# Kernel optimization log

Measured on AMD Instinct MI355X. Metric: run time of the kernel, lower is better.

Reference implementation:

```python
import jax, jax.numpy as jnp
import numpy as np


def setup_inputs() -> dict:
    key = jax.random.key(0)
    ks = jax.random.split(key, 8)
    B, dz, K, N, dx, T = 64, 16, 16, 1024, 128, 500
    # initial latent state [n_trials, dz, k_particles]
    z0 = jax.random.normal(ks[0], (B, dz, K), jnp.float32)
    # per-latent leak/time-constant A = (1 - dt/tau), kept in (0.8, 0.99) for stability
    A = jax.random.uniform(ks[1], (dz,), jnp.float32, minval=0.8, maxval=0.99)
    # low-rank recurrent factors: n [dz, N] (right), m [N, dz] (left)
    n = jax.random.normal(ks[2], (dz, N), jnp.float32) * (1.0 / N)
    m = jax.random.normal(ks[3], (N, dz), jnp.float32) * (1.0 / np.sqrt(dz))
    # neuron bias h [N], latent bias hz [dz]
    h = jax.random.normal(ks[4], (N,), jnp.float32) * 0.1
    hz = jax.random.normal(ks[5], (dz,), jnp.float32) * 0.01
    # readout B [dz, dx] ~ sqrt(2/dy) randn, bias initialised to zero (as in Observation)
    Bobs = jax.random.normal(ks[6], (dz, dx), jnp.float32) * np.sqrt(2.0 / dz)
    Bias = jnp.zeros((dx,), jnp.float32)
    return {"z0": z0, "A": A, "n": n, "m": m, "h": h, "hz": hz,
            "Bobs": Bobs, "Bias": Bias, "T": T}


def reference(z0, A, n, m, h, hz, Bobs, Bias, T):
    """Low-rank RNN rolled out for T steps + linear (identity-nonlin) readout.

    Per step (Transition.forward with relu nonlinearity, weight_scaler=1, du=0):
        R   = relu(m @ z - h)                       # rates, [B, N, K]
        z'  = A * z + n @ R + hz                    # [B, dz, K]
    Readout (Observation.forward, identity nonlinearity):
        X = einsum('zx,bzTK->bxTK', Bobs, zs) + Bias
    """
    Ab = A[None, :, None]      # [1, dz, 1]
    hb = h[None, :, None]      # [1, N, 1]
    hzb = hz[None, :, None]    # [1, dz, 1]

    def step(z, _):
        X = jnp.einsum('Nz,bzk->bNk', m, z)           # project to neurons
        R = jax.nn.relu(X - hb)                       # rates
        z_new = Ab * z + jnp.einsum('zN,bNk->bzk', n, R) + hzb
        return z_new, z_new

    _, zs = jax.lax.scan(step, z0, None, length=T)    # [T, B, dz, K]
    zs = jnp.transpose(zs, (1, 2, 0, 3))              # [B, dz, T, K]
    # Observation readout
    X = jnp.einsum('zx,bzTK->bxTK', Bobs, zs) + Bias[None, :, None, None]
    return X
```

## Files before the change

kernel.cpp:

```cpp
#include <hip/hip_runtime.h>
#include <hip/hip_bf16.h>


typedef __attribute__((ext_vector_type(4))) short short4v;
typedef __attribute__((ext_vector_type(8))) short short8v;
typedef __attribute__((ext_vector_type(4))) float float4v;

#define BB 64
#define DZ 16
#define KC 16
#define NN 1024
#define DX 128
#define NW 8
#define ITER (NN / (16 * NW))
#define NH (ITER / 2)
#define CH 8

union FragAB {
  short4v s;
  __hip_bfloat162 h2[2];
};
union Frag8 {
  short8v s8;
  short4v s4[2];
};

__device__ inline short4v pack_bf16x4(float a, float b, float c, float d) {
  FragAB u;
  u.h2[0] = __float22bfloat162_rn(make_float2(a, b));
  u.h2[1] = __float22bfloat162_rn(make_float2(c, d));
  return u.s;
}

__device__ inline float4v mfma_bf16(short4v a, short4v b, float4v c) {
#if __has_builtin(__builtin_amdgcn_mfma_f32_16x16x16bf16_1k)
  return __builtin_amdgcn_mfma_f32_16x16x16bf16_1k(a, b, c, 0, 0, 0);
#elif __has_builtin(__builtin_amdgcn_mfma_f32_16x16x16_bf16)
  return __builtin_amdgcn_mfma_f32_16x16x16_bf16(a, b, c, 0, 0, 0);
#else
  float4v d;
  asm("v_mfma_f32_16x16x16_bf16 %0, %1, %2, %3"
      : "=v"(d) : "v"(a), "v"(b), "v"(c));
  return d;
#endif
}

__device__ inline float4v mfma_bf16_x32(short8v a, short8v b, float4v c) {
#if __has_builtin(__builtin_amdgcn_mfma_f32_16x16x32_bf16)
  return __builtin_amdgcn_mfma_f32_16x16x32_bf16(a, b, c, 0, 0, 0);
#else
  float4v d;
  asm("v_mfma_f32_16x16x32_bf16 %0, %1, %2, %3"
      : "=v"(d) : "v"(a), "v"(b), "v"(c));
  return d;
#endif
}

__global__ __launch_bounds__(64 * NW, 2)
void lrrnn_fused(const float* __restrict__ z0, const float* __restrict__ Adec,
                 const float* __restrict__ nmat, const float* __restrict__ mmat,
                 const float* __restrict__ hvec, const float* __restrict__ hzvec,
                 const float* __restrict__ Bobs, const float* __restrict__ Bias,
                 const int* __restrict__ Tptr, float* __restrict__ out)
{
  const int T    = Tptr[0];
  const int b    = blockIdx.x;
  const int tid  = threadIdx.x;
  const int wave = tid >> 6;
  const int lane = tid & 63;
  const int g    = lane >> 4;
  const int c    = lane & 15;

  __shared__ float4v part[NW][64];
  __shared__ short4v zbuf[64];

  FragAB mf[ITER];
  Frag8  nf8[NH];
  float4v negH[ITER];
#pragma unroll
  for (int i = 0; i < ITER; ++i) {
    const int rowbase = wave * (16 * ITER) + i * 16;
    float4v mv = *(const float4v*)(mmat + (rowbase + c) * DZ + g * 4);
    mf[i].s = pack_bf16x4(mv[0], mv[1], mv[2], mv[3]);
    float4v hv = *(const float4v*)(hvec + rowbase + g * 4);
    negH[i][0] = -hv[0]; negH[i][1] = -hv[1];
    negH[i][2] = -hv[2]; negH[i][3] = -hv[3];
  }
#pragma unroll
  for (int i = 0; i < NH; ++i) {
    const int rb0 = wave * (16 * ITER) + (2 * i) * 16;
    float4v nv0 = *(const float4v*)(nmat + c * NN + rb0 + g * 4);
    float4v nv1 = *(const float4v*)(nmat + c * NN + rb0 + 16 + g * 4);
    nf8[i].s4[0] = pack_bf16x4(nv0[0], nv0[1], nv0[2], nv0[3]);
    nf8[i].s4[1] = pack_bf16x4(nv1[0], nv1[1], nv1[2], nv1[3]);
  }

  const float4v Af  = *(const float4v*)(Adec + g * 4);
  const float4v hzf = *(const float4v*)(hzvec + g * 4);
  const float4v zerov = {0.f, 0.f, 0.f, 0.f};

  FragAB bobsF;
  float4v biasF;
  unsigned oof[4];
  {
    const int xb = wave * 16;
    bobsF.s = pack_bf16x4(Bobs[(4 * g + 0) * DX + xb + c],
                          Bobs[(4 * g + 1) * DX + xb + c],
                          Bobs[(4 * g + 2) * DX + xb + c],
                          Bobs[(4 * g + 3) * DX + xb + c]);
    biasF = *(const float4v*)(Bias + xb + g * 4);
#pragma unroll
    for (int rr = 0; rr < 4; ++rr) {
      const int x = xb + g * 4 + rr;
      oof[rr] = (unsigned)(b * DX + x) * (unsigned)T * KC + c;
    }
  }

  float4v zf;
#pragma unroll
  for (int j = 0; j < 4; ++j)
    zf[j] = z0[b * DZ * KC + (g * 4 + j) * KC + c];
  FragAB zb;
  zb.s = pack_bf16x4(zf[0], zf[1], zf[2], zf[3]);

  auto do_step = [&]() {
    float4v xv[ITER];
#pragma unroll
    for (int i = 0; i < ITER; ++i)
      xv[i] = mfma_bf16(mf[i].s, zb.s, negH[i]);

    Frag8 R8[NH];
#pragma unroll
    for (int i = 0; i < NH; ++i) {
      const float4v x0 = xv[2 * i], x1 = xv[2 * i + 1];
      R8[i].s4[0] = pack_bf16x4(fmaxf(x0[0], 0.f), fmaxf(x0[1], 0.f),
                                fmaxf(x0[2], 0.f), fmaxf(x0[3], 0.f));
      R8[i].s4[1] = pack_bf16x4(fmaxf(x1[0], 0.f), fmaxf(x1[1], 0.f),
                                fmaxf(x1[2], 0.f), fmaxf(x1[3], 0.f));
    }

    float4v a0 = mfma_bf16_x32(nf8[0].s8, R8[0].s8, (wave == 0) ? hzf : zerov);
    float4v a1 = mfma_bf16_x32(nf8[1].s8, R8[1].s8, zerov);
    a0 = mfma_bf16_x32(nf8[2].s8, R8[2].s8, a0);
    a1 = mfma_bf16_x32(nf8[3].s8, R8[3].s8, a1);
    const float4v zp = a0 + a1;

    part[wave][lane] = zp;
    __syncthreads();

    if (wave == 0) {
      const float4v p1 = part[1][lane];
      const float4v p2 = part[2][lane];
      const float4v p3 = part[3][lane];
      const float4v p4 = part[4][lane];
      const float4v p5 = part[5][lane];
      const float4v p6 = part[6][lane];
      const float4v p7 = part[7][lane];
      const float4v tot = ((zp + p1) + (p2 + p3)) + ((p4 + p5) + (p6 + p7));
#pragma unroll
      for (int j = 0; j < 4; ++j)
        zf[j] = fmaf(Af[j], zf[j], tot[j]);
      zb.s = pack_bf16x4(zf[0], zf[1], zf[2], zf[3]);
      zbuf[lane] = zb.s;
    }
    __syncthreads();

    if (wave != 0) zb.s = zbuf[lane];
  };

  int t = 0;
  while (t + CH <= T) {
    short4v hist[CH];
#pragma unroll
    for (int s = 0; s < CH; ++s) {
      do_step();
      hist[s] = zb.s;
    }
#pragma unroll
    for (int s = 0; s < CH; ++s) {
      float4v o = mfma_bf16(bobsF.s, hist[s], biasF);
      const unsigned tk = (unsigned)(t + s) * KC;
#pragma unroll
      for (int rr = 0; rr < 4; ++rr)
        out[oof[rr] + tk] = o[rr];
    }
    t += CH;
  }
  for (; t < T; ++t) {
    do_step();
    float4v o = mfma_bf16(bobsF.s, zb.s, biasF);
    const unsigned tk = (unsigned)t * KC;
#pragma unroll
    for (int rr = 0; rr < 4; ++rr)
      out[oof[rr] + tk] = o[rr];
  }
}

extern "C" void kernel_launch(void* const* d_in, const int* in_sizes, int n_in,
                              void* d_out, int out_size, void* d_ws, size_t ws_size,
                              hipStream_t stream) {
  const float* z0   = (const float*)d_in[0];
  const float* A    = (const float*)d_in[1];
  const float* nmat = (const float*)d_in[2];
  const float* mmat = (const float*)d_in[3];
  const float* h    = (const float*)d_in[4];
  const float* hz   = (const float*)d_in[5];
  const float* Bobs = (const float*)d_in[6];
  const float* Bias = (const float*)d_in[7];
  const int*   T    = (const int*)d_in[8];
  (void)in_sizes; (void)n_in; (void)out_size; (void)d_ws; (void)ws_size;
  lrrnn_fused<<<dim3(BB), dim3(64 * NW), 0, stream>>>(
      z0, A, nmat, mmat, h, hz, Bobs, Bias, T, (float*)d_out);
}
```

Before: 343.9 us.

## Replace two-barrier reduction with redundant all-wave reduction and double-buffered partials

Every wave now reads all eight partial sums from shared memory and computes the updated latent state itself, instead of wave 0 reducing and broadcasting through a second shared buffer. Double-buffering the partial array lets each step use a single barrier rather than two. The decay and bias term is computed before the MFMA chain so it stays off the critical path. The cost is redundant LDS reads and adds in every wave, and the summation order changes slightly (hz is now added separately).

```diff
diff --git a/kernel.cpp b/kernel.cpp
--- a/kernel.cpp
+++ b/kernel.cpp
@@ -71,8 +71,7 @@
   const int g    = lane >> 4;
   const int c    = lane & 15;
 
-  __shared__ float4v part[NW][64];
-  __shared__ short4v zbuf[64];
+  __shared__ float4v part[2][NW][64];
 
   FragAB mf[ITER];
   Frag8  nf8[NH];
@@ -123,7 +122,12 @@
   FragAB zb;
   zb.s = pack_bf16x4(zf[0], zf[1], zf[2], zf[3]);
 
-  auto do_step = [&]() {
+  auto do_step = [&](int buf) {
+    float4v az;
+#pragma unroll
+    for (int j = 0; j < 4; ++j)
+      az[j] = fmaf(Af[j], zf[j], hzf[j]);
+
     float4v xv[ITER];
 #pragma unroll
     for (int i = 0; i < ITER; ++i)
@@ -139,33 +143,27 @@
                                 fmaxf(x1[2], 0.f), fmaxf(x1[3], 0.f));
     }
 
-    float4v a0 = mfma_bf16_x32(nf8[0].s8, R8[0].s8, (wave == 0) ? hzf : zerov);
+    float4v a0 = mfma_bf16_x32(nf8[0].s8, R8[0].s8, zerov);
     float4v a1 = mfma_bf16_x32(nf8[1].s8, R8[1].s8, zerov);
     a0 = mfma_bf16_x32(nf8[2].s8, R8[2].s8, a0);
     a1 = mfma_bf16_x32(nf8[3].s8, R8[3].s8, a1);
-    const float4v zp = a0 + a1;
-
-    part[wave][lane] = zp;
+
+    part[buf][wave][lane] = a0 + a1;
     __syncthreads();
 
-    if (wave == 0) {
-      const float4v p1 = part[1][lane];
-      const float4v p2 = part[2][lane];
-      const float4v p3 = part[3][lane];
-      const float4v p4 = part[4][lane];
-      const float4v p5 = part[5][lane];
-      const float4v p6 = part[6][lane];
-      const float4v p7 = part[7][lane];
-      const float4v tot = ((zp + p1) + (p2 + p3)) + ((p4 + p5) + (p6 + p7));
-#pragma unroll
-      for (int j = 0; j < 4; ++j)
-        zf[j] = fmaf(Af[j], zf[j], tot[j]);
-      zb.s = pack_bf16x4(zf[0], zf[1], zf[2], zf[3]);
-      zbuf[lane] = zb.s;
-    }
-    __syncthreads();
-
-    if (wave != 0) zb.s = zbuf[lane];
+    const float4v p0 = part[buf][0][lane];
+    const float4v p1 = part[buf][1][lane];
+    const float4v p2 = part[buf][2][lane];
+    const float4v p3 = part[buf][3][lane];
+    const float4v p4 = part[buf][4][lane];
+    const float4v p5 = part[buf][5][lane];
+    const float4v p6 = part[buf][6][lane];
+    const float4v p7 = part[buf][7][lane];
+    const float4v tot = ((p0 + p1) + (p2 + p3)) + ((p4 + p5) + (p6 + p7));
+#pragma unroll
+    for (int j = 0; j < 4; ++j)
+      zf[j] = az[j] + tot[j];
+    zb.s = pack_bf16x4(zf[0], zf[1], zf[2], zf[3]);
   };
 
   int t = 0;
@@ -173,7 +171,7 @@
     short4v hist[CH];
 #pragma unroll
     for (int s = 0; s < CH; ++s) {
-      do_step();
+      do_step(s & 1);
       hist[s] = zb.s;
     }
 #pragma unroll
@@ -187,7 +185,7 @@
     t += CH;
   }
   for (; t < T; ++t) {
-    do_step();
+    do_step(t & 1);
     float4v o = mfma_bf16(bobsF.s, zb.s, biasF);
     const unsigned tk = (unsigned)t * KC;
 #pragma unroll
```

New measurement: 388.6 us. +13.0%, slower.

## Replace per-step block barriers with LDS flag-based producer/consumer handoff

Applied to the files above, without the earlier changes.

Removes the two __syncthreads per recurrence step. Worker waves now publish their partial sums and set a 16-bit step flag in shared memory, then spin until wave 0 posts the new latent state with its own step flag. Wave 0 polls the packed partial flags, reduces, writes the bf16 state and sets the flag. This is meant to cut barrier latency on the serial 500-step critical path. The cost is spinning waves taking issue slots, plus reliance on LDS ordering done by hand with s_waitcnt and volatile accesses.

```diff
diff --git a/kernel.cpp b/kernel.cpp
--- a/kernel.cpp
+++ b/kernel.cpp
@@ -73,6 +73,12 @@
 
   __shared__ float4v part[NW][64];
   __shared__ short4v zbuf[64];
+  __shared__ unsigned zflag[64];
+  __shared__ unsigned short pflags[8];
+
+  if (tid < 64) zflag[tid] = 0u;
+  if (tid < 8)  pflags[tid] = 0;
+  __syncthreads();
 
   FragAB mf[ITER];
   Frag8  nf8[NH];
@@ -123,7 +129,9 @@
   FragAB zb;
   zb.s = pack_bf16x4(zf[0], zf[1], zf[2], zf[3]);
 
-  auto do_step = [&]() {
+  auto do_step = [&](int t) {
+    const unsigned want = (unsigned)t + 1u;
+
     float4v xv[ITER];
 #pragma unroll
     for (int i = 0; i < ITER; ++i)
@@ -145,10 +153,25 @@
     a1 = mfma_bf16_x32(nf8[3].s8, R8[3].s8, a1);
     const float4v zp = a0 + a1;
 
-    part[wave][lane] = zp;
-    __syncthreads();
-
-    if (wave == 0) {
+    if (wave != 0) {
+      part[wave][lane] = zp;
+      asm volatile("s_waitcnt lgkmcnt(0)" ::: "memory");
+      if (lane == 0)
+        ((volatile unsigned short*)pflags)[wave] = (unsigned short)want;
+
+      while (((const volatile unsigned*)zflag)[lane] != want) {}
+      asm volatile("" ::: "memory");
+      zb.s = zbuf[lane];
+    } else {
+      if (lane == 0)
+        ((volatile unsigned short*)pflags)[0] = (unsigned short)want;
+      const unsigned want2 = (want & 0xffffu) | (want << 16);
+      const volatile unsigned* pf = (const volatile unsigned*)pflags;
+      for (;;) {
+        const unsigned f0 = pf[0], f1 = pf[1], f2 = pf[2], f3 = pf[3];
+        if (f0 == want2 && f1 == want2 && f2 == want2 && f3 == want2) break;
+      }
+      asm volatile("" ::: "memory");
       const float4v p1 = part[1][lane];
       const float4v p2 = part[2][lane];
       const float4v p3 = part[3][lane];
@@ -162,10 +185,9 @@
         zf[j] = fmaf(Af[j], zf[j], tot[j]);
       zb.s = pack_bf16x4(zf[0], zf[1], zf[2], zf[3]);
       zbuf[lane] = zb.s;
-    }
-    __syncthreads();
-
-    if (wave != 0) zb.s = zbuf[lane];
+      asm volatile("s_waitcnt lgkmcnt(0)" ::: "memory");
+      ((volatile unsigned*)zflag)[lane] = want;
+    }
   };
 
   int t = 0;
@@ -173,7 +195,7 @@
     short4v hist[CH];
 #pragma unroll
     for (int s = 0; s < CH; ++s) {
-      do_step();
+      do_step(t + s);
       hist[s] = zb.s;
     }
 #pragma unroll
@@ -187,7 +209,7 @@
     t += CH;
   }
   for (; t < T; ++t) {
-    do_step();
+    do_step(t);
     float4v o = mfma_bf16(bobsF.s, zb.s, biasF);
     const unsigned tk = (unsigned)t * KC;
 #pragma unroll
```

After: 449.5 us. 1.31x slower.
